# Optimization experiments

Hardware: AMD Instinct MI355X
Metric: run time of the kernel (lower is better)

The kernel has to match this reference:

```python
import jax, jax.numpy as jnp
import numpy as np

N = 262144          # anchors per batch (dense detector)
C = 80              # COCO classes; targets==C means background/negative
ALPHA = 0.25
GAMMA = 2.0
LOSS_WEIGHT = 1.0
MAX_SCHEMA = 65536  # schema ints kept < 2**16 so float32 holds them exactly


def setup_inputs() -> dict:
    key = jax.random.key(0)
    k1, k2, k3 = jax.random.split(key, 3)
    pred = jax.random.normal(k1, (N, C), dtype=jnp.float32)
    targets = jax.random.randint(k2, (N,), 0, C + 1, dtype=jnp.int32)
    weight = jax.random.randint(k3, (N,), 0, MAX_SCHEMA, dtype=jnp.int32).astype(jnp.float32)
    return {"pred": pred, "targets": targets, "weight": weight}


def reference(pred, targets, weight):
    num_classes = pred.shape[1]
    # --- vectorized cross_mask: bit-unpack schema for negative rows ---
    # cur_schema (reversed binary string) => bit c of int(schema)
    wint = weight.astype(jnp.int32)
    bits = ((wint[:, None] >> jnp.arange(num_classes, dtype=jnp.int32)[None, :]) & 1).astype(pred.dtype)  # (N,C)
    neg = (targets == num_classes)[:, None]                       # (N,1) negative rows
    cross_mask = jnp.where(neg, bits, jnp.ones((), pred.dtype))   # (N,C)
    # --- sigmoid focal loss (mmcv semantics: target==c is positive; target==C -> all-zero one-hot) ---
    onehot = jax.nn.one_hot(targets, num_classes, dtype=pred.dtype)  # (N,C); bg row is all zeros
    p = jax.nn.sigmoid(pred)
    pt = onehot * (1.0 - p) + (1.0 - onehot) * p
    focal_w = (ALPHA * onehot + (1.0 - ALPHA) * (1.0 - onehot)) * pt ** GAMMA
    # stable BCE-with-logits: -log sigmoid(x) = softplus(-x)
    bce = onehot * jax.nn.softplus(-pred) + (1.0 - onehot) * jax.nn.softplus(pred)
    # use_weight=True: weight binarized to {0,1} per row
    w = jnp.where(weight > 0, 1.0, 0.0).astype(pred.dtype)[:, None]
    loss = focal_w * bce * w * cross_mask
    return LOSS_WEIGHT * loss.mean()
```

## Files before the change

### kernel.cpp

```cpp
#include <hip/hip_runtime.h>
#include <hip/hip_bf16.h>


#define NCLS 80
#define C4   (NCLS / 4)
#define NBLOCKS 2048
#define NTHREADS 256
#define STRIDE (NBLOCKS * NTHREADS)

__device__ __forceinline__ float log1p_poly(float x) {
    float p = -0.0064535442f;
    p = __builtin_fmaf(p, x,  0.0360884937f);
    p = __builtin_fmaf(p, x, -0.0953293897f);
    p = __builtin_fmaf(p, x,  0.1676540711f);
    p = __builtin_fmaf(p, x, -0.2407338084f);
    p = __builtin_fmaf(p, x,  0.3317990258f);
    p = __builtin_fmaf(p, x, -0.4998741238f);
    p = __builtin_fmaf(p, x,  0.9999964239f);
    return p * x;
}

__device__ __forceinline__ float elem_term(float x, int c, int t, int wi, bool neg) {
    const bool  pos = (c == t);
    const int   bit = (c < 32) ? ((wi >> c) & 1) : 0;
    const float m   = neg ? (float)bit : 1.0f;
    const float a   = pos ? 0.25f : 0.75f;
    const float y   = pos ? -x : x;
    const float e   = __expf(-fabsf(y));
    const float inv = __builtin_amdgcn_rcpf(1.0f + e);
    const float s   = (y >= 0.0f) ? inv : e * inv;
    const float sp  = fmaxf(y, 0.0f) + log1p_poly(e);
    return (a * m) * (s * s) * sp;
}

__device__ __forceinline__ float body(const float* __restrict__ pred,
                                      const int*   __restrict__ targets,
                                      const float* __restrict__ weight,
                                      int i) {
    const int n  = i / C4;
    const int r  = i - n * C4;
    const int c0 = r * 4;

    const float4 x4 = reinterpret_cast<const float4*>(pred)[i];
    const int    t  = targets[n];
    const float  wf = weight[n];
    const int    wi = (int)wf;
    const bool  neg = (t == NCLS);
    const float  rw = (wf > 0.0f) ? 1.0f : 0.0f;

    const float s4 = elem_term(x4.x, c0 + 0, t, wi, neg)
                   + elem_term(x4.y, c0 + 1, t, wi, neg)
                   + elem_term(x4.z, c0 + 2, t, wi, neg)
                   + elem_term(x4.w, c0 + 3, t, wi, neg);
    return rw * s4;
}

template<int KITERS>
__global__ void __launch_bounds__(NTHREADS)
cfs_main(const float* __restrict__ pred,
         const int*   __restrict__ targets,
         const float* __restrict__ weight,
         float* __restrict__ partials,
         int total4) {
    const int tid = blockIdx.x * NTHREADS + threadIdx.x;

    float acc = 0.0f;
    if constexpr (KITERS > 0) {
        #pragma unroll
        for (int k = 0; k < KITERS; ++k)
            acc += body(pred, targets, weight, tid + k * STRIDE);
    } else {
        for (int i = tid; i < total4; i += STRIDE)
            acc += body(pred, targets, weight, i);
    }

    #pragma unroll
    for (int off = 32; off > 0; off >>= 1)
        acc += __shfl_down(acc, off, 64);

    __shared__ float smem[NTHREADS / 64];
    const int lane = threadIdx.x & 63;
    const int wid  = threadIdx.x >> 6;
    if (lane == 0) smem[wid] = acc;
    __syncthreads();
    if (threadIdx.x == 0) {
        float v = 0.0f;
        #pragma unroll
        for (int w = 0; w < NTHREADS / 64; ++w) v += smem[w];
        partials[blockIdx.x] = v;
    }
}

__global__ void __launch_bounds__(NTHREADS)
cfs_reduce(const float* __restrict__ partials, float* __restrict__ out,
           int nparts, float scale) {
    float acc = 0.0f;
    for (int i = threadIdx.x; i < nparts; i += NTHREADS)
        acc += partials[i];
    #pragma unroll
    for (int off = 32; off > 0; off >>= 1)
        acc += __shfl_down(acc, off, 64);

    __shared__ float smem[NTHREADS / 64];
    const int lane = threadIdx.x & 63;
    const int wid  = threadIdx.x >> 6;
    if (lane == 0) smem[wid] = acc;
    __syncthreads();
    if (threadIdx.x == 0) {
        float v = 0.0f;
        #pragma unroll
        for (int w = 0; w < NTHREADS / 64; ++w) v += smem[w];
        out[0] = v * scale;
    }
}

extern "C" void kernel_launch(void* const* d_in, const int* in_sizes, int n_in,
                              void* d_out, int out_size, void* d_ws, size_t ws_size,
                              hipStream_t stream) {
    const float* pred     = (const float*)d_in[0];
    const int*   targets  = (const int*)  d_in[1];
    const float* weight   = (const float*)d_in[2];
    float*       out      = (float*)d_out;
    float*       partials = (float*)d_ws;

    const int n_rows = in_sizes[1];
    const int total4 = n_rows * C4;
    const float inv_total = 1.0f / (float)(n_rows * NCLS);

    if (total4 == 10 * STRIDE) {
        cfs_main<10><<<NBLOCKS, NTHREADS, 0, stream>>>(pred, targets, weight, partials, total4);
    } else {
        cfs_main<0><<<NBLOCKS, NTHREADS, 0, stream>>>(pred, targets, weight, partials, total4);
    }
    cfs_reduce<<<1, NTHREADS, 0, stream>>>(partials, out, NBLOCKS, inv_total);
}
```

Baseline: 27.46 us.

## Fuse final reduction into main kernel via last-block atomic counter

Removes the separate single-block reduce kernel: each block stores its partial, bumps an atomic counter, and the last block to finish sums all partials and writes the output. This saves one kernel launch and its dependency gap, but adds a memset of the counter on the stream. The pred loads also become nontemporal vector loads so streaming data bypasses cache retention, and exp now takes |x| directly instead of |y| (the same value, so one negation is dropped).

New measurement: 108.3 us. 3.94x slower.

```diff
diff --git a/kernel.cpp b/kernel.cpp
--- a/kernel.cpp
+++ b/kernel.cpp
@@ -7,6 +7,8 @@
 #define NBLOCKS 2048
 #define NTHREADS 256
 #define STRIDE (NBLOCKS * NTHREADS)
+
+typedef float f32x4 __attribute__((ext_vector_type(4)));
 
 __device__ __forceinline__ float log1p_poly(float x) {
     float p = -0.0064535442f;
@@ -26,7 +28,7 @@
     const float m   = neg ? (float)bit : 1.0f;
     const float a   = pos ? 0.25f : 0.75f;
     const float y   = pos ? -x : x;
-    const float e   = __expf(-fabsf(y));
+    const float e   = __expf(-fabsf(x));
     const float inv = __builtin_amdgcn_rcpf(1.0f + e);
     const float s   = (y >= 0.0f) ? inv : e * inv;
     const float sp  = fmaxf(y, 0.0f) + log1p_poly(e);
@@ -41,27 +43,29 @@
     const int r  = i - n * C4;
     const int c0 = r * 4;
 
-    const float4 x4 = reinterpret_cast<const float4*>(pred)[i];
+    const f32x4 x4 = __builtin_nontemporal_load(reinterpret_cast<const f32x4*>(pred) + i);
     const int    t  = targets[n];
     const float  wf = weight[n];
     const int    wi = (int)wf;
     const bool  neg = (t == NCLS);
     const float  rw = (wf > 0.0f) ? 1.0f : 0.0f;
 
-    const float s4 = elem_term(x4.x, c0 + 0, t, wi, neg)
-                   + elem_term(x4.y, c0 + 1, t, wi, neg)
-                   + elem_term(x4.z, c0 + 2, t, wi, neg)
-                   + elem_term(x4.w, c0 + 3, t, wi, neg);
+    const float s4 = elem_term(x4[0], c0 + 0, t, wi, neg)
+                   + elem_term(x4[1], c0 + 1, t, wi, neg)
+                   + elem_term(x4[2], c0 + 2, t, wi, neg)
+                   + elem_term(x4[3], c0 + 3, t, wi, neg);
     return rw * s4;
 }
 
 template<int KITERS>
 __global__ void __launch_bounds__(NTHREADS)
-cfs_main(const float* __restrict__ pred,
-         const int*   __restrict__ targets,
-         const float* __restrict__ weight,
-         float* __restrict__ partials,
-         int total4) {
+cfs_fused(const float* __restrict__ pred,
+          const int*   __restrict__ targets,
+          const float* __restrict__ weight,
+          float* __restrict__ partials,
+          unsigned* __restrict__ counter,
+          float* __restrict__ out,
+          int total4, float scale) {
     const int tid = blockIdx.x * NTHREADS + threadIdx.x;
 
     float acc = 0.0f;
@@ -79,38 +83,40 @@
         acc += __shfl_down(acc, off, 64);
 
     __shared__ float smem[NTHREADS / 64];
+    __shared__ int lastFlag;
     const int lane = threadIdx.x & 63;
     const int wid  = threadIdx.x >> 6;
     if (lane == 0) smem[wid] = acc;
     __syncthreads();
+
     if (threadIdx.x == 0) {
         float v = 0.0f;
         #pragma unroll
         for (int w = 0; w < NTHREADS / 64; ++w) v += smem[w];
-        partials[blockIdx.x] = v;
+        __hip_atomic_store(&partials[blockIdx.x], v, __ATOMIC_RELAXED, __HIP_MEMORY_SCOPE_AGENT);
+        __threadfence();
+        const unsigned ret = __hip_atomic_fetch_add(counter, 1u, __ATOMIC_RELAXED,
+                                                    __HIP_MEMORY_SCOPE_AGENT);
+        lastFlag = (ret == NBLOCKS - 1);
     }
-}
+    __syncthreads();
 
-__global__ void __launch_bounds__(NTHREADS)
-cfs_reduce(const float* __restrict__ partials, float* __restrict__ out,
-           int nparts, float scale) {
-    float acc = 0.0f;
-    for (int i = threadIdx.x; i < nparts; i += NTHREADS)
-        acc += partials[i];
-    #pragma unroll
-    for (int off = 32; off > 0; off >>= 1)
-        acc += __shfl_down(acc, off, 64);
-
-    __shared__ float smem[NTHREADS / 64];
-    const int lane = threadIdx.x & 63;
-    const int wid  = threadIdx.x >> 6;
-    if (lane == 0) smem[wid] = acc;
-    __syncthreads();
-    if (threadIdx.x == 0) {
-        float v = 0.0f;
+    if (lastFlag) {
+        __threadfence();
+        float a2 = 0.0f;
+        for (int i = threadIdx.x; i < NBLOCKS; i += NTHREADS)
+            a2 += __hip_atomic_load(&partials[i], __ATOMIC_RELAXED, __HIP_MEMORY_SCOPE_AGENT);
         #pragma unroll
-        for (int w = 0; w < NTHREADS / 64; ++w) v += smem[w];
-        out[0] = v * scale;
+        for (int off = 32; off > 0; off >>= 1)
+            a2 += __shfl_down(a2, off, 64);
+        if (lane == 0) smem[wid] = a2;
+        __syncthreads();
+        if (threadIdx.x == 0) {
+            float v = 0.0f;
+            #pragma unroll
+            for (int w = 0; w < NTHREADS / 64; ++w) v += smem[w];
+            out[0] = v * scale;
+        }
     }
 }
 
@@ -122,15 +128,21 @@
     const float* weight   = (const float*)d_in[2];
     float*       out      = (float*)d_out;
     float*       partials = (float*)d_ws;
+    unsigned*    counter  = (unsigned*)((char*)d_ws + NBLOCKS * sizeof(float));
 
     const int n_rows = in_sizes[1];
     const int total4 = n_rows * C4;
     const float inv_total = 1.0f / (float)(n_rows * NCLS);
 
+    (void)hipMemsetAsync(counter, 0, sizeof(unsigned), stream);
+
     if (total4 == 10 * STRIDE) {
-        cfs_main<10><<<NBLOCKS, NTHREADS, 0, stream>>>(pred, targets, weight, partials, total4);
+        cfs_fused<10><<<NBLOCKS, NTHREADS, 0, stream>>>(pred, targets, weight,
+                                                        partials, counter, out,
+                                                        total4, inv_total);
     } else {
-        cfs_main<0><<<NBLOCKS, NTHREADS, 0, stream>>>(pred, targets, weight, partials, total4);
+        cfs_fused<0><<<NBLOCKS, NTHREADS, 0, stream>>>(pred, targets, weight,
+                                                       partials, counter, out,
+                                                       total4, inv_total);
     }
-    cfs_reduce<<<1, NTHREADS, 0, stream>>>(partials, out, NBLOCKS, inv_total);
 }
```
